# Performance work log

Measured on AMD Instinct MI355X. Metric: run time of the kernel, lower is better.

The kernel has to match this reference:

```python
import jax, jax.numpy as jnp
import numpy as np


def setup_inputs() -> dict:
    key = jax.random.key(0)
    k1, k2, k3 = jax.random.split(key, 3)
    B, gd, gh, gw = 4, 8, 16, 16
    H, W = 1024, 1024
    grid = jax.random.normal(k1, (B, 12, gd, gh, gw), dtype=jnp.float32)
    guide = jax.random.uniform(k2, (B, H, W), dtype=jnp.float32)
    image = jax.random.uniform(k3, (B, 3, H, W), dtype=jnp.float32)
    return {"grid": grid, "guide": guide, "image": image}


def _slice_apply(grid, guide, image):
    # grid: [B, 12, gd, gh, gw]; guide: [B, H, W] in [0,1]; image: [B, 3, H, W]
    B, C, gd, gh, gw = grid.shape
    _, h, w = guide.shape
    dt = grid.dtype
    # continuous grid coordinates (Halide reference convention)
    gx = (jnp.arange(w, dtype=dt) + 0.5) * gw / w          # [w]
    gy = (jnp.arange(h, dtype=dt) + 0.5) * gh / h          # [h]
    gz = guide * gd                                        # [B,h,w]
    fx = jnp.floor(gx - 0.5)
    fy = jnp.floor(gy - 0.5)
    fz = jnp.floor(gz - 0.5)
    bidx = jnp.arange(B)[:, None, None]
    coeffs = jnp.zeros((B, h, w, C), dt)
    # 8-corner trilinear gather with tent weights (clamped borders)
    for dz in (0, 1):
        zf = fz + dz
        wz = jnp.maximum(1.0 - jnp.abs(zf + 0.5 - gz), 0.0)       # [B,h,w]
        iz = jnp.clip(zf, 0, gd - 1).astype(jnp.int32)
        for dy in (0, 1):
            yf = fy + dy
            wy = jnp.maximum(1.0 - jnp.abs(yf + 0.5 - gy), 0.0)   # [h]
            iy = jnp.clip(yf, 0, gh - 1).astype(jnp.int32)
            for dx in (0, 1):
                xf = fx + dx
                wx = jnp.maximum(1.0 - jnp.abs(xf + 0.5 - gx), 0.0)  # [w]
                ix = jnp.clip(xf, 0, gw - 1).astype(jnp.int32)
                # gather -> [B,h,w,C]
                g = grid[bidx, :, iz, iy[None, :, None], ix[None, None, :]]
                wgt = wz * wy[None, :, None] * wx[None, None, :]
                coeffs = coeffs + g * wgt[..., None]
    # per-pixel 3x4 affine transform: out_i = sum_j A_ij * in_j + b_i
    co = coeffs.reshape(B, h, w, 3, 4)
    out = jnp.einsum('bhwij,bjhw->bihw', co[..., :3], image) + co[..., 3].transpose(0, 3, 1, 2)
    return out


def reference(grid, guide, image):
    return _slice_apply(grid, guide, image)
```

## Files before the change

kernel.cpp:

```cpp
#include <hip/hip_runtime.h>
#include <hip/hip_fp16.h>

#define IMH 1024
#define IMW 1024
#define GD 8
#define GH 16
#define GW 16
#define NC 12
#define NZB 7
#define ENT 24
#define ROWS 4

__global__ __launch_bounds__(256) void bsa_kernel(
    const float* __restrict__ grid,
    const float* __restrict__ guide,
    const float* __restrict__ image,
    float* __restrict__ out)
{
    const int y0  = blockIdx.x * ROWS;
    const int b   = blockIdx.y;
    const int tid = threadIdx.x;

    __shared__ __align__(16) __half sH[2][GW][NZB][ENT];
    __half* const sbase = &sH[0][0][0][0];
    const int SBUF = GW * NZB * ENT;

    const float* gb = grid + (size_t)b * NC * GD * GH * GW;

    int gsrc[6], sx[6], sz[6], sc[6];
    #pragma unroll
    for (int k = 0; k < 6; ++k) {
        const int i = tid + 256 * k;
        sx[k] = i & (GW - 1);
        sz[k] = (i >> 4) & (GD - 1);
        sc[k] = i >> 7;
        gsrc[k] = ((sc[k] * GD + sz[k]) * GH) * GW + sx[k];
    }

    int   xo0[4], xo1[4];
    float wx0v[4], wx1v[4];
    #pragma unroll
    for (int p = 0; p < 4; ++p) {
        const int   x   = tid + 256 * p;
        const float gx  = (x + 0.5f) * ((float)GW / IMW);
        const float fxf = floorf(gx - 0.5f);
        const float tx  = gx - 0.5f - fxf;
        const int   fx  = (int)fxf;
        const int   ix0 = min(GW - 1, max(0, fx));
        const int   ix1 = min(GW - 1, max(0, fx + 1));
        xo0[p] = ix0 * (NZB * ENT);
        xo1[p] = ix1 * (NZB * ENT);
        wx0v[p] = 1.0f - tx;
        wx1v[p] = tx;
    }

    {
        const float gy  = (y0 + 0.5f) * ((float)GH / IMH);
        const float fyf = floorf(gy - 0.5f);
        const float ty  = gy - 0.5f - fyf;
        const int   fy  = (int)fyf;
        const int   iy0 = min(GH - 1, max(0, fy));
        const int   iy1 = min(GH - 1, max(0, fy + 1));
        #pragma unroll
        for (int k = 0; k < 6; ++k) {
            const float v0 = gb[gsrc[k] + iy0 * GW];
            const float v1 = gb[gsrc[k] + iy1 * GW];
            const __half h = __float2half(v0 + ty * (v1 - v0));
            const int x = sx[k], z = sz[k], c = sc[k];
            if (z < NZB) sH[0][x][z][c] = h;
            if (z > 0)   sH[0][x][z - 1][NC + c] = h;
        }
    }
    __syncthreads();

    const size_t plane = (size_t)IMH * IMW;

    #pragma unroll
    for (int j = 0; j < ROWS; ++j) {
        float nv0[6], nv1[6], nty = 0.0f;
        if (j + 1 < ROWS) {
            const int   yn  = y0 + j + 1;
            const float gy  = (yn + 0.5f) * ((float)GH / IMH);
            const float fyf = floorf(gy - 0.5f);
            nty = gy - 0.5f - fyf;
            const int fy  = (int)fyf;
            const int iy0 = min(GH - 1, max(0, fy));
            const int iy1 = min(GH - 1, max(0, fy + 1));
            #pragma unroll
            for (int k = 0; k < 6; ++k) {
                nv0[k] = gb[gsrc[k] + iy0 * GW];
                nv1[k] = gb[gsrc[k] + iy1 * GW];
            }
        }

        const int y = y0 + j;
        const float* gp = guide + ((size_t)b * IMH + y) * IMW;
        const float* ip = image + ((size_t)b * 3 * IMH + y) * IMW;
        float*       op = out   + ((size_t)b * 3 * IMH + y) * IMW;
        const __half* S = sbase + (j & 1) * SBUF;

        #pragma unroll
        for (int p = 0; p < 4; ++p) {
            const int x = tid + 256 * p;

            const float gv = gp[x];
            const float rv = ip[x];
            const float g2 = ip[x + plane];
            const float bv = ip[x + 2 * plane];

            const float gz  = gv * (float)GD;
            const float fzf = floorf(gz - 0.5f);
            const float tz  = gz - 0.5f - fzf;
            const int   fzi = (int)fzf;
            const int   zb  = min(NZB - 1, max(0, fzi));
            const float az  = (fzi < 0) ? 1.0f : ((fzi > NZB - 1) ? 0.0f : 1.0f - tz);
            const float bz  = (fzi < 0) ? 0.0f : ((fzi > NZB - 1) ? 1.0f : tz);

            const __half2 wa0 = __float2half2_rn(az * wx0v[p]);
            const __half2 wb0 = __float2half2_rn(bz * wx0v[p]);
            const __half2 wa1 = __float2half2_rn(az * wx1v[p]);
            const __half2 wb1 = __float2half2_rn(bz * wx1v[p]);

            const __half* e0 = S + xo0[p] + zb * ENT;
            const __half* e1 = S + xo1[p] + zb * ENT;

            __half2 A[12], B[12];
            *(uint4*)(A + 0) = *(const uint4*)(e0);
            *(uint4*)(A + 4) = *(const uint4*)(e0 + 8);
            *(uint4*)(A + 8) = *(const uint4*)(e0 + 16);
            *(uint4*)(B + 0) = *(const uint4*)(e1);
            *(uint4*)(B + 4) = *(const uint4*)(e1 + 8);
            *(uint4*)(B + 8) = *(const uint4*)(e1 + 16);

            __half2 cl[6];
            #pragma unroll
            for (int d = 0; d < 6; ++d) {
                __half2 t = __hmul2(wa0, A[d]);
                t = __hfma2(wb0, A[d + 6], t);
                t = __hfma2(wa1, B[d], t);
                t = __hfma2(wb1, B[d + 6], t);
                cl[d] = t;
            }

            float res[3];
            #pragma unroll
            for (int i = 0; i < 3; ++i) {
                const float c0 = __low2float(cl[2 * i]);
                const float c1 = __high2float(cl[2 * i]);
                const float c2 = __low2float(cl[2 * i + 1]);
                const float c3 = __high2float(cl[2 * i + 1]);
                res[i] = fmaf(c0, rv, fmaf(c1, g2, fmaf(c2, bv, c3)));
            }

            op[x]             = res[0];
            op[x + plane]     = res[1];
            op[x + 2 * plane] = res[2];
        }

        if (j + 1 < ROWS) {
            __half* D = sbase + ((j + 1) & 1) * SBUF;
            #pragma unroll
            for (int k = 0; k < 6; ++k) {
                const __half h = __float2half(nv0[k] + nty * (nv1[k] - nv0[k]));
                const int x = sx[k], z = sz[k], c = sc[k];
                if (z < NZB) D[(x * NZB + z) * ENT + c] = h;
                if (z > 0)   D[(x * NZB + (z - 1)) * ENT + NC + c] = h;
            }
        }
        __syncthreads();
    }
}

extern "C" void kernel_launch(void* const* d_in, const int* in_sizes, int n_in,
                              void* d_out, int out_size, void* d_ws, size_t ws_size,
                              hipStream_t stream) {
    const float* grid  = (const float*)d_in[0];
    const float* guide = (const float*)d_in[1];
    const float* image = (const float*)d_in[2];
    float* out = (float*)d_out;

    const int B = in_sizes[1] / (IMH * IMW);
    dim3 g(IMH / ROWS, B);
    bsa_kernel<<<g, 256, 0, stream>>>(grid, guide, image, out);
}
```

Before: 121.1 us.

## Precompute all row slices into shared memory up front and drop per-row barriers

After: 114.4 us. 1.06x faster.

```diff
diff --git a/kernel.cpp b/kernel.cpp
--- a/kernel.cpp
+++ b/kernel.cpp
@@ -11,7 +11,7 @@
 #define ENT 24
 #define ROWS 4
 
-__global__ __launch_bounds__(256) void bsa_kernel(
+__global__ __launch_bounds__(256, 4) void bsa_kernel(
     const float* __restrict__ grid,
     const float* __restrict__ guide,
     const float* __restrict__ image,
@@ -21,21 +21,9 @@
     const int b   = blockIdx.y;
     const int tid = threadIdx.x;
 
-    __shared__ __align__(16) __half sH[2][GW][NZB][ENT];
-    __half* const sbase = &sH[0][0][0][0];
-    const int SBUF = GW * NZB * ENT;
+    __shared__ __align__(16) __half sH[ROWS][GW][NZB][ENT];
 
     const float* gb = grid + (size_t)b * NC * GD * GH * GW;
-
-    int gsrc[6], sx[6], sz[6], sc[6];
-    #pragma unroll
-    for (int k = 0; k < 6; ++k) {
-        const int i = tid + 256 * k;
-        sx[k] = i & (GW - 1);
-        sz[k] = (i >> 4) & (GD - 1);
-        sc[k] = i >> 7;
-        gsrc[k] = ((sc[k] * GD + sz[k]) * GH) * GW + sx[k];
-    }
 
     int   xo0[4], xo1[4];
     float wx0v[4], wx1v[4];
@@ -46,29 +34,49 @@
         const float fxf = floorf(gx - 0.5f);
         const float tx  = gx - 0.5f - fxf;
         const int   fx  = (int)fxf;
-        const int   ix0 = min(GW - 1, max(0, fx));
-        const int   ix1 = min(GW - 1, max(0, fx + 1));
-        xo0[p] = ix0 * (NZB * ENT);
-        xo1[p] = ix1 * (NZB * ENT);
+        xo0[p] = min(GW - 1, max(0, fx)) * (NZB * ENT);
+        xo1[p] = min(GW - 1, max(0, fx + 1)) * (NZB * ENT);
         wx0v[p] = 1.0f - tx;
         wx1v[p] = tx;
     }
 
     {
-        const float gy  = (y0 + 0.5f) * ((float)GH / IMH);
-        const float fyf = floorf(gy - 0.5f);
-        const float ty  = gy - 0.5f - fyf;
-        const int   fy  = (int)fyf;
+        const int q  = tid >> 1;
+        const int x  = q & (GW - 1);
+        const int z  = q >> 4;
+        const int c0 = (tid & 1) * 6;
+
+        const float gy0 = (y0 + 0.5f) * ((float)GH / IMH);
+        const int   fy  = (int)floorf(gy0 - 0.5f);
         const int   iy0 = min(GH - 1, max(0, fy));
         const int   iy1 = min(GH - 1, max(0, fy + 1));
+
+        float v0[6], v1[6];
         #pragma unroll
-        for (int k = 0; k < 6; ++k) {
-            const float v0 = gb[gsrc[k] + iy0 * GW];
-            const float v1 = gb[gsrc[k] + iy1 * GW];
-            const __half h = __float2half(v0 + ty * (v1 - v0));
-            const int x = sx[k], z = sz[k], c = sc[k];
-            if (z < NZB) sH[0][x][z][c] = h;
-            if (z > 0)   sH[0][x][z - 1][NC + c] = h;
+        for (int c = 0; c < 6; ++c) {
+            const int cc = c0 + c;
+            v0[c] = gb[((cc * GD + z) * GH + iy0) * GW + x];
+            v1[c] = gb[((cc * GD + z) * GH + iy1) * GW + x];
+        }
+
+        #pragma unroll
+        for (int r = 0; r < ROWS; ++r) {
+            const float ty = (y0 + r + 0.5f) * ((float)GH / IMH) - 0.5f - (float)fy;
+            __half2 hv[3];
+            #pragma unroll
+            for (int d = 0; d < 3; ++d) {
+                const float a = v0[2*d]   + ty * (v1[2*d]   - v0[2*d]);
+                const float c = v0[2*d+1] + ty * (v1[2*d+1] - v0[2*d+1]);
+                hv[d] = __halves2half2(__float2half(a), __float2half(c));
+            }
+            if (z < NZB) {
+                __half2* dst = (__half2*)&sH[r][x][z][c0];
+                dst[0] = hv[0]; dst[1] = hv[1]; dst[2] = hv[2];
+            }
+            if (z > 0) {
+                __half2* dst = (__half2*)&sH[r][x][z - 1][NC + c0];
+                dst[0] = hv[0]; dst[1] = hv[1]; dst[2] = hv[2];
+            }
         }
     }
     __syncthreads();
@@ -76,28 +84,12 @@
     const size_t plane = (size_t)IMH * IMW;
 
     #pragma unroll
-    for (int j = 0; j < ROWS; ++j) {
-        float nv0[6], nv1[6], nty = 0.0f;
-        if (j + 1 < ROWS) {
-            const int   yn  = y0 + j + 1;
-            const float gy  = (yn + 0.5f) * ((float)GH / IMH);
-            const float fyf = floorf(gy - 0.5f);
-            nty = gy - 0.5f - fyf;
-            const int fy  = (int)fyf;
-            const int iy0 = min(GH - 1, max(0, fy));
-            const int iy1 = min(GH - 1, max(0, fy + 1));
-            #pragma unroll
-            for (int k = 0; k < 6; ++k) {
-                nv0[k] = gb[gsrc[k] + iy0 * GW];
-                nv1[k] = gb[gsrc[k] + iy1 * GW];
-            }
-        }
-
-        const int y = y0 + j;
+    for (int r = 0; r < ROWS; ++r) {
+        const int y = y0 + r;
         const float* gp = guide + ((size_t)b * IMH + y) * IMW;
         const float* ip = image + ((size_t)b * 3 * IMH + y) * IMW;
         float*       op = out   + ((size_t)b * 3 * IMH + y) * IMW;
-        const __half* S = sbase + (j & 1) * SBUF;
+        const __half* S = &sH[r][0][0][0];
 
         #pragma unroll
         for (int p = 0; p < 4; ++p) {
@@ -145,29 +137,17 @@
             float res[3];
             #pragma unroll
             for (int i = 0; i < 3; ++i) {
-                const float c0 = __low2float(cl[2 * i]);
-                const float c1 = __high2float(cl[2 * i]);
-                const float c2 = __low2float(cl[2 * i + 1]);
-                const float c3 = __high2float(cl[2 * i + 1]);
-                res[i] = fmaf(c0, rv, fmaf(c1, g2, fmaf(c2, bv, c3)));
+                const float c0f = __low2float(cl[2 * i]);
+                const float c1f = __high2float(cl[2 * i]);
+                const float c2f = __low2float(cl[2 * i + 1]);
+                const float c3f = __high2float(cl[2 * i + 1]);
+                res[i] = fmaf(c0f, rv, fmaf(c1f, g2, fmaf(c2f, bv, c3f)));
             }
 
             op[x]             = res[0];
             op[x + plane]     = res[1];
             op[x + 2 * plane] = res[2];
         }
-
-        if (j + 1 < ROWS) {
-            __half* D = sbase + ((j + 1) & 1) * SBUF;
-            #pragma unroll
-            for (int k = 0; k < 6; ++k) {
-                const __half h = __float2half(nv0[k] + nty * (nv1[k] - nv0[k]));
-                const int x = sx[k], z = sz[k], c = sc[k];
-                if (z < NZB) D[(x * NZB + z) * ENT + c] = h;
-                if (z > 0)   D[(x * NZB + (z - 1)) * ENT + NC + c] = h;
-            }
-        }
-        __syncthreads();
     }
 }
 
```
